# Performance work log

Hardware: AMD Instinct MI355X
Metric: run time of the kernel (lower is better)

Reference implementation:

```python
import jax, jax.numpy as jnp
import numpy as np

MARGIN = 1.0

def setup_inputs() -> dict:
    key = jax.random.key(0)
    k1, k2, k3 = jax.random.split(key, 3)
    B, C, D = 65536, 1000, 512
    x = jax.random.normal(k1, (B, D), dtype=jnp.float32)
    x = x / jnp.linalg.norm(x, axis=1, keepdims=True)  # docstring: ||x||2 = 1
    labels = jax.random.randint(k2, (B,), 0, C, dtype=jnp.int64)
    centers = jax.random.normal(k3, (C, D), dtype=jnp.float32)
    return {"x": x, "labels": labels, "centers": centers}

def reference(x, labels, centers):
    # l2Norm applied to the centers (module is only used when l2Norm is truthy)
    c = centers / jnp.linalg.norm(centers, axis=1, keepdims=True)  # (C, D)
    # cosine distance to every center: one batched GEMM instead of per-sample loop
    dist = 1.0 - jnp.einsum("bd,cd->bc", x, c)                      # (B, C)
    pos = jnp.take_along_axis(dist, labels[:, None], axis=1)[:, 0]  # (B,)
    # min over all classes != label: mask own class with +inf
    same = jnp.arange(c.shape[0])[None, :] == labels[:, None]       # (B, C)
    neg = jnp.min(jnp.where(same, jnp.inf, dist), axis=1)           # (B,)
    # sum of per-sample hinge losses divided by batch size == mean
    return jnp.mean(jax.nn.relu(pos + MARGIN - neg))
```

## Files before the change

### kernel.cpp

```cpp
#include <hip/hip_runtime.h>
#include <stdint.h>

typedef short v8s __attribute__((ext_vector_type(8)));
typedef short v4s __attribute__((ext_vector_type(4)));
typedef float v4f __attribute__((ext_vector_type(4)));

#define BM 256
#define BN 128
#define BK 64
#define POS_INF __builtin_inff()

typedef __attribute__((address_space(3))) unsigned int lds_uint;
typedef const __attribute__((address_space(1))) unsigned int glb_uint;

__device__ __forceinline__ void load16_lds(const void* g, void* l) {
    __builtin_amdgcn_global_load_lds((glb_uint*)g, (lds_uint*)l, 16, 0, 0);
}

__device__ __forceinline__ short f2bf(float f) {
    uint32_t u = __builtin_bit_cast(uint32_t, f);
    u += 0x7fffu + ((u >> 16) & 1u);
    return (short)(u >> 16);
}

__global__ void prep(const float* __restrict__ centers,
                     unsigned short* __restrict__ cbf,
                     int C, int D, int CP, int CB,
                     const float* __restrict__ x,
                     unsigned short* __restrict__ xbf, size_t nx,
                     int* __restrict__ cnt, int NB,
                     float* __restrict__ out) {
    const int b = blockIdx.x;
    const int t = threadIdx.x;
    if (b == 0 && t == 0) out[0] = 0.0f;
    if (b < CB) {
        const int g = b * 256 + t;
        if (g < NB) cnt[g] = 0;
        const int wave = t >> 6, lane = t & 63;
        const int row = b * 4 + wave;
        if (row >= CP) return;
        if (row >= C) {
            v4s z = {0, 0, 0, 0};
            for (int d = lane * 4; d < D; d += 256)
                *(v4s*)&cbf[(size_t)row * D + d] = z;
            return;
        }
        const float* src = centers + (size_t)row * D;
        float ss = 0.0f;
        for (int d = lane * 4; d < D; d += 256) {
            v4f f = *(const v4f*)&src[d];
            ss += f.x * f.x + f.y * f.y + f.z * f.z + f.w * f.w;
        }
        #pragma unroll
        for (int off = 32; off; off >>= 1) ss += __shfl_xor(ss, off, 64);
        const float rn = rsqrtf(ss);
        for (int d = lane * 4; d < D; d += 256) {
            v4f f = *(const v4f*)&src[d];
            v4s s;
            s.x = f2bf(f.x * rn); s.y = f2bf(f.y * rn);
            s.z = f2bf(f.z * rn); s.w = f2bf(f.w * rn);
            *(v4s*)&cbf[(size_t)row * D + d] = s;
        }
    } else {
        const size_t i = ((size_t)(b - CB) * 256 + t) * 8;
        if (i >= nx) return;
        v4f f0 = *(const v4f*)&x[i];
        v4f f1 = *(const v4f*)&x[i + 4];
        v8s s;
        s[0] = f2bf(f0.x); s[1] = f2bf(f0.y); s[2] = f2bf(f0.z); s[3] = f2bf(f0.w);
        s[4] = f2bf(f1.x); s[5] = f2bf(f1.y); s[6] = f2bf(f1.z); s[7] = f2bf(f1.w);
        *(v8s*)&xbf[i] = s;
    }
}

__global__ void __launch_bounds__(512)
gemm_fused(const unsigned short* __restrict__ xbf,
           const unsigned short* __restrict__ cbf,
           const int* __restrict__ labels,
           float* __restrict__ pos, float* __restrict__ partial,
           int* __restrict__ cnt,
           int Bt, int C, int D, int NT, float margin,
           float* __restrict__ out) {
    __shared__ short LDSbuf[(BM + BN) * BK];
    short* As = LDSbuf;
    short* Bs = LDSbuf + BM * BK;

    const int t   = threadIdx.x;
    const int bid = blockIdx.x;
    const int xcd = bid & 7;
    const int per = bid >> 3;
    const int rowblk = (per >> 3) * 8 + xcd;
    const int nt     = per & 7;
    const int row0 = rowblk * BM;
    const int n0   = nt * BN;

    const int lane = t & 63;
    const int wave = t >> 6;
    const int wm = wave >> 1;
    const int wn = wave & 1;
    const int l15 = lane & 15, q = lane >> 4;

    const int rsub = lane >> 3;
    const int csrc = (lane & 7) ^ rsub;

    int myLab = 0;
    if (t < BM) myLab = labels[row0 + t];

    v4f acc[4][4];
    #pragma unroll
    for (int i = 0; i < 4; ++i)
        #pragma unroll
        for (int j = 0; j < 4; ++j)
            acc[i][j] = (v4f){0.f, 0.f, 0.f, 0.f};

    const int KT = D / BK;
    for (int kk = 0; kk < KT; ++kk) {
        const int k0 = kk * BK;
        #pragma unroll
        for (int p = 0; p < 4; ++p) {
            const int rbase = wave * 32 + p * 8;
            const unsigned short* g =
                &xbf[(size_t)(row0 + rbase + rsub) * D + k0 + csrc * 8];
            load16_lds(g, &As[rbase * BK]);
        }
        #pragma unroll
        for (int p = 0; p < 2; ++p) {
            const int rbase = wave * 16 + p * 8;
            const unsigned short* g =
                &cbf[(size_t)(n0 + rbase + rsub) * D + k0 + csrc * 8];
            load16_lds(g, &Bs[rbase * BK]);
        }
        __syncthreads();
        #pragma unroll
        for (int ki = 0; ki < BK; ki += 32) {
            const int cbase = ki >> 3;
            v8s a[4], b[4];
            #pragma unroll
            for (int i = 0; i < 4; ++i) {
                const int m = wm * 64 + i * 16 + l15;
                a[i] = *(const v8s*)&As[m * BK + (((cbase + q) ^ (l15 & 7)) * 8)];
            }
            #pragma unroll
            for (int j = 0; j < 4; ++j) {
                const int n = wn * 64 + j * 16 + l15;
                b[j] = *(const v8s*)&Bs[n * BK + (((cbase + q) ^ (l15 & 7)) * 8)];
            }
            #pragma unroll
            for (int i = 0; i < 4; ++i)
                #pragma unroll
                for (int j = 0; j < 4; ++j)
                    acc[i][j] = __builtin_amdgcn_mfma_f32_16x16x32_bf16(
                        a[i], b[j], acc[i][j], 0, 0, 0);
        }
        __syncthreads();
    }

    int*   Ls    = (int*)As;
    float* sMinW = (float*)Bs;
    int*   sLast = (int*)(Bs + 2 * BM * 2);
    float* wsum  = (float*)(sLast + 1);
    if (t < BM) Ls[t] = myLab;
    __syncthreads();

    #pragma unroll
    for (int i = 0; i < 4; ++i) {
        #pragma unroll
        for (int rg = 0; rg < 4; ++rg) {
            const int row_l = wm * 64 + i * 16 + q * 4 + rg;
            const int lab = Ls[row_l];
            float m = POS_INF;
            #pragma unroll
            for (int j = 0; j < 4; ++j) {
                const int col = n0 + wn * 64 + j * 16 + l15;
                const float d = 1.0f - acc[i][j][rg];
                if (col == lab)
                    __hip_atomic_store(&pos[row0 + row_l], d,
                                       __ATOMIC_RELAXED, __HIP_MEMORY_SCOPE_AGENT);
                else if (col < C) m = fminf(m, d);
            }
            m = fminf(m, __shfl_xor(m, 1, 64));
            m = fminf(m, __shfl_xor(m, 2, 64));
            m = fminf(m, __shfl_xor(m, 4, 64));
            m = fminf(m, __shfl_xor(m, 8, 64));
            if (l15 == 0) sMinW[wn * BM + row_l] = m;
        }
    }
    __syncthreads();
    if (t < BM) {
        const float m = fminf(sMinW[t], sMinW[BM + t]);
        __hip_atomic_store(&partial[(size_t)nt * Bt + row0 + t], m,
                           __ATOMIC_RELAXED, __HIP_MEMORY_SCOPE_AGENT);
    }
    __syncthreads();

    if (t == 0) {
        __builtin_amdgcn_s_waitcnt(0);
        const int old = __hip_atomic_fetch_add(&cnt[rowblk], 1,
                                               __ATOMIC_RELAXED,
                                               __HIP_MEMORY_SCOPE_AGENT);
        *sLast = (old == NT - 1);
    }
    __syncthreads();
    if (!*sLast) return;

    float hng = 0.0f;
    if (t < BM) {
        const int r = row0 + t;
        float neg = POS_INF;
        for (int tt = 0; tt < NT; ++tt)
            neg = fminf(neg, __hip_atomic_load(&partial[(size_t)tt * Bt + r],
                                               __ATOMIC_RELAXED,
                                               __HIP_MEMORY_SCOPE_AGENT));
        const float p = __hip_atomic_load(&pos[r], __ATOMIC_RELAXED,
                                          __HIP_MEMORY_SCOPE_AGENT);
        hng = fmaxf(0.0f, p + margin - neg);
    }
    #pragma unroll
    for (int off = 32; off; off >>= 1) hng += __shfl_down(hng, off, 64);
    if (lane == 0) wsum[wave] = hng;
    __syncthreads();
    if (t == 0) {
        float s = 0.0f;
        #pragma unroll
        for (int w = 0; w < 8; ++w) s += wsum[w];
        atomicAdd(out, s * (1.0f / (float)Bt));
    }
}

extern "C" void kernel_launch(void* const* d_in, const int* in_sizes, int n_in,
                              void* d_out, int out_size, void* d_ws, size_t ws_size,
                              hipStream_t stream) {
    const float* x       = (const float*)d_in[0];
    const int*   labels  = (const int*)d_in[1];
    const float* centers = (const float*)d_in[2];
    float* out = (float*)d_out;

    const int Bt = in_sizes[1];
    const int D  = in_sizes[0] / Bt;
    const int C  = in_sizes[2] / D;
    const int NT = (C + BN - 1) / BN;
    const int CP = NT * BN;
    const int NB = Bt / BM;

    char* ws = (char*)d_ws;
    unsigned short* cbf = (unsigned short*)ws;
    size_t off = (size_t)CP * D * 2;
    off = (off + 255) & ~(size_t)255;
    float* pos = (float*)(ws + off);      off += (size_t)Bt * 4;
    float* partial = (float*)(ws + off);  off += (size_t)NT * Bt * 4;
    int* cnt = (int*)(ws + off);          off += (size_t)NB * 4;
    off = (off + 255) & ~(size_t)255;
    unsigned short* xbf = (unsigned short*)(ws + off);

    const size_t nx = (size_t)Bt * D;
    const int CB = CP / 4;
    const int XB = (int)((nx / 8 + 255) / 256);
    prep<<<CB + XB, 256, 0, stream>>>(centers, cbf, C, D, CP, CB, x, xbf, nx,
                                      cnt, NB, out);

    gemm_fused<<<NB * NT, 512, 0, stream>>>(xbf, cbf, labels, pos, partial, cnt,
                                            Bt, C, D, NT, 1.0f, out);
}
```

Measured before the change: 290.2 us.

## Fuse x bf16 conversion into GEMM by loading fp32 x into LDS

```diff
diff --git a/kernel.cpp b/kernel.cpp
--- a/kernel.cpp
+++ b/kernel.cpp
@@ -25,65 +25,53 @@
 
 __global__ void prep(const float* __restrict__ centers,
                      unsigned short* __restrict__ cbf,
-                     int C, int D, int CP, int CB,
-                     const float* __restrict__ x,
-                     unsigned short* __restrict__ xbf, size_t nx,
+                     int C, int D, int CP,
                      int* __restrict__ cnt, int NB,
                      float* __restrict__ out) {
     const int b = blockIdx.x;
     const int t = threadIdx.x;
     if (b == 0 && t == 0) out[0] = 0.0f;
-    if (b < CB) {
+    {
         const int g = b * 256 + t;
         if (g < NB) cnt[g] = 0;
-        const int wave = t >> 6, lane = t & 63;
-        const int row = b * 4 + wave;
-        if (row >= CP) return;
-        if (row >= C) {
-            v4s z = {0, 0, 0, 0};
-            for (int d = lane * 4; d < D; d += 256)
-                *(v4s*)&cbf[(size_t)row * D + d] = z;
-            return;
-        }
-        const float* src = centers + (size_t)row * D;
-        float ss = 0.0f;
-        for (int d = lane * 4; d < D; d += 256) {
-            v4f f = *(const v4f*)&src[d];
-            ss += f.x * f.x + f.y * f.y + f.z * f.z + f.w * f.w;
-        }
-        #pragma unroll
-        for (int off = 32; off; off >>= 1) ss += __shfl_xor(ss, off, 64);
-        const float rn = rsqrtf(ss);
-        for (int d = lane * 4; d < D; d += 256) {
-            v4f f = *(const v4f*)&src[d];
-            v4s s;
-            s.x = f2bf(f.x * rn); s.y = f2bf(f.y * rn);
-            s.z = f2bf(f.z * rn); s.w = f2bf(f.w * rn);
-            *(v4s*)&cbf[(size_t)row * D + d] = s;
-        }
-    } else {
-        const size_t i = ((size_t)(b - CB) * 256 + t) * 8;
-        if (i >= nx) return;
-        v4f f0 = *(const v4f*)&x[i];
-        v4f f1 = *(const v4f*)&x[i + 4];
-        v8s s;
-        s[0] = f2bf(f0.x); s[1] = f2bf(f0.y); s[2] = f2bf(f0.z); s[3] = f2bf(f0.w);
-        s[4] = f2bf(f1.x); s[5] = f2bf(f1.y); s[6] = f2bf(f1.z); s[7] = f2bf(f1.w);
-        *(v8s*)&xbf[i] = s;
+    }
+    const int wave = t >> 6, lane = t & 63;
+    const int row = b * 4 + wave;
+    if (row >= CP) return;
+    if (row >= C) {
+        v4s z = {0, 0, 0, 0};
+        for (int d = lane * 4; d < D; d += 256)
+            *(v4s*)&cbf[(size_t)row * D + d] = z;
+        return;
+    }
+    const float* src = centers + (size_t)row * D;
+    float ss = 0.0f;
+    for (int d = lane * 4; d < D; d += 256) {
+        v4f f = *(const v4f*)&src[d];
+        ss += f.x * f.x + f.y * f.y + f.z * f.z + f.w * f.w;
+    }
+    #pragma unroll
+    for (int off = 32; off; off >>= 1) ss += __shfl_xor(ss, off, 64);
+    const float rn = rsqrtf(ss);
+    for (int d = lane * 4; d < D; d += 256) {
+        v4f f = *(const v4f*)&src[d];
+        v4s s;
+        s.x = f2bf(f.x * rn); s.y = f2bf(f.y * rn);
+        s.z = f2bf(f.z * rn); s.w = f2bf(f.w * rn);
+        *(v4s*)&cbf[(size_t)row * D + d] = s;
     }
 }
 
 __global__ void __launch_bounds__(512)
-gemm_fused(const unsigned short* __restrict__ xbf,
+gemm_fused(const float* __restrict__ x,
            const unsigned short* __restrict__ cbf,
            const int* __restrict__ labels,
            float* __restrict__ pos, float* __restrict__ partial,
            int* __restrict__ cnt,
            int Bt, int C, int D, int NT, float margin,
            float* __restrict__ out) {
-    __shared__ short LDSbuf[(BM + BN) * BK];
-    short* As = LDSbuf;
-    short* Bs = LDSbuf + BM * BK;
+    __shared__ float Af[BM * BK];
+    __shared__ short Bs[BN * BK];
 
     const int t   = threadIdx.x;
     const int bid = blockIdx.x;
@@ -100,8 +88,10 @@
     const int wn = wave & 1;
     const int l15 = lane & 15, q = lane >> 4;
 
-    const int rsub = lane >> 3;
-    const int csrc = (lane & 7) ^ rsub;
+    const int rsubB = lane >> 3;
+    const int csrcB = (lane & 7) ^ rsubB;
+
+    const int rsubA = lane >> 4;
 
     int myLab = 0;
     if (t < BM) myLab = labels[row0 + t];
@@ -117,33 +107,48 @@
     for (int kk = 0; kk < KT; ++kk) {
         const int k0 = kk * BK;
         #pragma unroll
-        for (int p = 0; p < 4; ++p) {
-            const int rbase = wave * 32 + p * 8;
-            const unsigned short* g =
-                &xbf[(size_t)(row0 + rbase + rsub) * D + k0 + csrc * 8];
-            load16_lds(g, &As[rbase * BK]);
+        for (int p = 0; p < 8; ++p) {
+            const int rbase = wave * 32 + p * 4;
+            const int row = rbase + rsubA;
+            const int csrc = l15 ^ (row & 15);
+            const float* g = &x[(size_t)(row0 + row) * D + k0 + csrc * 4];
+            load16_lds(g, &Af[rbase * BK]);
         }
         #pragma unroll
         for (int p = 0; p < 2; ++p) {
             const int rbase = wave * 16 + p * 8;
             const unsigned short* g =
-                &cbf[(size_t)(n0 + rbase + rsub) * D + k0 + csrc * 8];
+                &cbf[(size_t)(n0 + rbase + rsubB) * D + k0 + csrcB * 8];
             load16_lds(g, &Bs[rbase * BK]);
         }
         __syncthreads();
         #pragma unroll
         for (int ki = 0; ki < BK; ki += 32) {
-            const int cbase = ki >> 3;
+            const int cbaseA = ki >> 2;
+            const int cbaseB = ki >> 3;
             v8s a[4], b[4];
             #pragma unroll
             for (int i = 0; i < 4; ++i) {
                 const int m = wm * 64 + i * 16 + l15;
-                a[i] = *(const v8s*)&As[m * BK + (((cbase + q) ^ (l15 & 7)) * 8)];
+                const int slot0 = (cbaseA + 2 * q) ^ l15;
+                const int slot1 = slot0 ^ 1;
+                v4f f0 = *(const v4f*)&Af[m * BK + slot0 * 4];
+                v4f f1 = *(const v4f*)&Af[m * BK + slot1 * 4];
+                unsigned short us[8];
+                us[0] = (unsigned short)(__builtin_bit_cast(uint32_t, f0.x) >> 16);
+                us[1] = (unsigned short)(__builtin_bit_cast(uint32_t, f0.y) >> 16);
+                us[2] = (unsigned short)(__builtin_bit_cast(uint32_t, f0.z) >> 16);
+                us[3] = (unsigned short)(__builtin_bit_cast(uint32_t, f0.w) >> 16);
+                us[4] = (unsigned short)(__builtin_bit_cast(uint32_t, f1.x) >> 16);
+                us[5] = (unsigned short)(__builtin_bit_cast(uint32_t, f1.y) >> 16);
+                us[6] = (unsigned short)(__builtin_bit_cast(uint32_t, f1.z) >> 16);
+                us[7] = (unsigned short)(__builtin_bit_cast(uint32_t, f1.w) >> 16);
+                a[i] = *(v8s*)us;
             }
             #pragma unroll
             for (int j = 0; j < 4; ++j) {
                 const int n = wn * 64 + j * 16 + l15;
-                b[j] = *(const v8s*)&Bs[n * BK + (((cbase + q) ^ (l15 & 7)) * 8)];
+                b[j] = *(const v8s*)&Bs[n * BK + (((cbaseB + q) ^ (l15 & 7)) * 8)];
             }
             #pragma unroll
             for (int i = 0; i < 4; ++i)
@@ -155,9 +160,9 @@
         __syncthreads();
     }
 
-    int*   Ls    = (int*)As;
+    int*   Ls    = (int*)Af;
     float* sMinW = (float*)Bs;
-    int*   sLast = (int*)(Bs + 2 * BM * 2);
+    int*   sLast = (int*)((char*)Bs + 2 * BM * 4);
     float* wsum  = (float*)(sLast + 1);
     if (t < BM) Ls[t] = myLab;
     __syncthreads();
@@ -248,16 +253,10 @@
     off = (off + 255) & ~(size_t)255;
     float* pos = (float*)(ws + off);      off += (size_t)Bt * 4;
     float* partial = (float*)(ws + off);  off += (size_t)NT * Bt * 4;
-    int* cnt = (int*)(ws + off);          off += (size_t)NB * 4;
-    off = (off + 255) & ~(size_t)255;
-    unsigned short* xbf = (unsigned short*)(ws + off);
-
-    const size_t nx = (size_t)Bt * D;
-    const int CB = CP / 4;
-    const int XB = (int)((nx / 8 + 255) / 256);
-    prep<<<CB + XB, 256, 0, stream>>>(centers, cbf, C, D, CP, CB, x, xbf, nx,
-                                      cnt, NB, out);
-
-    gemm_fused<<<NB * NT, 512, 0, stream>>>(xbf, cbf, labels, pos, partial, cnt,
+    int* cnt = (int*)(ws + off);
+
+    prep<<<CP / 4, 256, 0, stream>>>(centers, cbf, C, D, CP, cnt, NB, out);
+
+    gemm_fused<<<NB * NT, 512, 0, stream>>>(x, cbf, labels, pos, partial, cnt,
                                             Bt, C, D, NT, 1.0f, out);
 }
```

After: 374.3 us. 1.29x slower.
